# Kernel tuning notes

Measured on AMD Instinct MI355X. Metric: run time of the kernel, lower is better.

Reference implementation:

```python
import jax, jax.numpy as jnp
import numpy as np

B, N1, K, E, H = 64, 8, 128, 256, 512


def setup_inputs() -> dict:
    key = jax.random.key(0)
    ks = jax.random.split(key, 10)
    s = 1.0 / np.sqrt(E)
    sh = 1.0 / np.sqrt(H)
    return {
        "queries": jax.random.normal(ks[0], (B, N1, E), jnp.float32),
        "keys": jax.random.normal(ks[1], (B, N1, K, E), jnp.float32),
        "cum_subs_masks": jax.random.randint(ks[2], (B, N1, K, 1), 0, 2, jnp.int32),
        "num_neg": N1 - 1,
        "wk_w": jax.random.uniform(ks[3], (H, E), jnp.float32, -s, s),
        "wk_b": jax.random.uniform(ks[4], (H,), jnp.float32, -s, s),
        "wq_w": jax.random.uniform(ks[5], (H, E), jnp.float32, -s, s),
        "wq_b": jax.random.uniform(ks[6], (H,), jnp.float32, -s, s),
        "wv_w": jax.random.uniform(ks[7], (1, H), jnp.float32, -sh, sh),
        "wv_b": jax.random.uniform(ks[8], (1,), jnp.float32, -sh, sh),
    }


def reference(queries, keys, cum_subs_masks, num_neg, wk_w, wk_b, wq_w, wq_b, wv_w, wv_b):
    # queries: (B, N1, E) -> project and broadcast over keys dim
    q_proj = jnp.einsum("bne,he->bnh", queries, wq_w) + wq_b        # (B, N1, H)
    k_proj = jnp.einsum("bnke,he->bnkh", keys, wk_w) + wk_b          # (B, N1, K, H)
    hidden = jnp.tanh(q_proj[:, :, None, :] + k_proj)                # (B, N1, K, H)
    scores = jnp.einsum("bnkh,oh->bnko", hidden, wv_w) + wv_b        # (B, N1, K, 1)
    scores = scores + cum_subs_masks.astype(scores.dtype) * (-1e9)
    attn_weight = jax.nn.softmax(scores, axis=-2)                    # over K
    attn_out = jnp.sum(attn_weight * keys, axis=-2)                  # (B, N1, E)
    return attn_out, attn_weight
```

## Files before the change

### kernel.cpp

```cpp
#include <hip/hip_runtime.h>
#include <hip/hip_bf16.h>

#define B_  64
#define N1_ 8
#define KK  128
#define EE  256
#define HH  512
#define BN  (B_ * N1_)

typedef __attribute__((ext_vector_type(8))) short short8;
typedef __attribute__((ext_vector_type(4))) float f32x4;

__device__ __forceinline__ short bfs(float f) {
  __hip_bfloat16 h = __float2bfloat16(f);
  return __builtin_bit_cast(short, h);
}

__device__ __forceinline__ float tanhf_fast(float x) {
  float e2 = __builtin_amdgcn_exp2f(2.8853900817779268f * x);
  return 1.0f - 2.0f * __builtin_amdgcn_rcpf(e2 + 1.0f);
}

__device__ __forceinline__ void gload16(const void* g, void* l) {
  __builtin_amdgcn_global_load_lds(
      (const __attribute__((address_space(1))) void*)g,
      (__attribute__((address_space(3))) void*)l, 16, 0, 0);
}

__global__ __launch_bounds__(256) void k_prep(
    const float* __restrict__ wk_w,
    const float* __restrict__ queries,
    const float* __restrict__ wq_w,
    const float* __restrict__ wq_b,
    const float* __restrict__ wk_b,
    unsigned short* __restrict__ wk_fr,
    float* __restrict__ qp) {
  const int bid = blockIdx.x, t = threadIdx.x;
  if (bid < 64) {
    const int g  = bid * 256 + t;
    const int h  = g >> 5;
    const int e0 = (g & 31) * 8;
    float4 x = *(const float4*)(wk_w + (size_t)h * EE + e0);
    float4 y = *(const float4*)(wk_w + (size_t)h * EE + e0 + 4);
    short8 f;
    f[0] = bfs(x.x); f[1] = bfs(x.y); f[2] = bfs(x.z); f[3] = bfs(x.w);
    f[4] = bfs(y.x); f[5] = bfs(y.y); f[6] = bfs(y.z); f[7] = bfs(y.w);
    const int ht = h >> 4, hl = h & 15;
    const int s = e0 >> 5, lg = (e0 >> 3) & 3;
    const int chunk = (ht * 8 + s) * 64 + lg * 16 + hl;
    *(short8*)(wk_fr + (size_t)chunk * 8) = f;
  } else {
    const int w = t >> 6, l = t & 63, lg = l >> 4, ll = l & 15;
    const int g2 = bid - 64;
    const int bn0 = (g2 >> 1) * 16;
    const int ht0 = (g2 & 1) * 16;
    short8 af[8];
    {
      const float* qr = queries + (size_t)(bn0 + ll) * EE + lg * 8;
      #pragma unroll
      for (int s = 0; s < 8; ++s) {
        float4 x = *(const float4*)(qr + s * 32);
        float4 y = *(const float4*)(qr + s * 32 + 4);
        short8 f;
        f[0] = bfs(x.x); f[1] = bfs(x.y); f[2] = bfs(x.z); f[3] = bfs(x.w);
        f[4] = bfs(y.x); f[5] = bfs(y.y); f[6] = bfs(y.z); f[7] = bfs(y.w);
        af[s] = f;
      }
    }
    #pragma unroll
    for (int i = 0; i < 4; ++i) {
      const int ht = ht0 + w * 4 + i;
      const float* bp = wq_w + (size_t)(ht * 16 + ll) * EE + lg * 8;
      f32x4 a = {0.f, 0.f, 0.f, 0.f};
      #pragma unroll
      for (int s = 0; s < 8; ++s) {
        float4 x = *(const float4*)(bp + s * 32);
        float4 y = *(const float4*)(bp + s * 32 + 4);
        short8 f;
        f[0] = bfs(x.x); f[1] = bfs(x.y); f[2] = bfs(x.z); f[3] = bfs(x.w);
        f[4] = bfs(y.x); f[5] = bfs(y.y); f[6] = bfs(y.z); f[7] = bfs(y.w);
        a = __builtin_amdgcn_mfma_f32_16x16x32_bf16(af[s], f, a, 0, 0, 0);
      }
      const int h = ht * 16 + ll;
      const float add = wq_b[h] + wk_b[h];
      #pragma unroll
      for (int r = 0; r < 4; ++r)
        qp[(size_t)(bn0 + lg * 4 + r) * HH + h] = a[r] + add;
    }
  }
}

__global__ __launch_bounds__(256, 2) void k_fused(
    const float* __restrict__ keys,
    const unsigned short* __restrict__ wk_fr,
    const float* __restrict__ wv_w,
    const float* __restrict__ qp,
    const int* __restrict__ masks,
    float* __restrict__ out) {
  const int t  = threadIdx.x;
  const int w  = t >> 6;
  const int l  = t & 63;
  const int lg = l >> 4;
  const int ll = l & 15;
  const int bn = blockIdx.x;

  __shared__ __align__(16) char bsm[2][8192];
  __shared__ float qb_s[HH];
  __shared__ float wv_s[HH];
  __shared__ float sc[KK];
  __shared__ float red[2];
  __shared__ float4 po4[4][64];

  qb_s[t]       = qp[(size_t)bn * HH + t];
  qb_s[t + 256] = qp[(size_t)bn * HH + t + 256];
  wv_s[t]       = wv_w[t];
  wv_s[t + 256] = wv_w[t + 256];

  const char* wkb = (const char*)wk_fr;
  gload16(wkb + (size_t)t * 16,        &bsm[0][w * 1024]);
  gload16(wkb + 4096 + (size_t)t * 16, &bsm[0][4096 + w * 1024]);

  short8 af0[8], af1[8];
  {
    const float* kp0 = keys + (size_t)(bn * KK + w * 32 + ll) * EE + lg * 8;
    const float* kp1 = kp0 + 16 * EE;
    #pragma unroll
    for (int s = 0; s < 8; ++s) {
      float4 x = *(const float4*)(kp0 + s * 32);
      float4 y = *(const float4*)(kp0 + s * 32 + 4);
      short8 f;
      f[0] = bfs(x.x); f[1] = bfs(x.y); f[2] = bfs(x.z); f[3] = bfs(x.w);
      f[4] = bfs(y.x); f[5] = bfs(y.y); f[6] = bfs(y.z); f[7] = bfs(y.w);
      af0[s] = f;
      x = *(const float4*)(kp1 + s * 32);
      y = *(const float4*)(kp1 + s * 32 + 4);
      f[0] = bfs(x.x); f[1] = bfs(x.y); f[2] = bfs(x.z); f[3] = bfs(x.w);
      f[4] = bfs(y.x); f[5] = bfs(y.y); f[6] = bfs(y.z); f[7] = bfs(y.w);
      af1[s] = f;
    }
  }
  __syncthreads();

  float p0[4] = {0.f, 0.f, 0.f, 0.f};
  float p1[4] = {0.f, 0.f, 0.f, 0.f};

  for (int i = 0; i < 32; ++i) {
    if (i < 31) {
      const char* src = wkb + (size_t)(i + 1) * 8192 + (size_t)t * 16;
      char* dst = &bsm[(i + 1) & 1][w * 1024];
      gload16(src, dst);
      gload16(src + 4096, dst + 4096);
    }
    const char* buf = bsm[i & 1];
    f32x4 a0 = {0.f, 0.f, 0.f, 0.f};
    f32x4 a1 = {0.f, 0.f, 0.f, 0.f};
    #pragma unroll
    for (int s = 0; s < 8; ++s) {
      short8 bfr = *(const short8*)(buf + s * 1024 + l * 16);
      a0 = __builtin_amdgcn_mfma_f32_16x16x32_bf16(af0[s], bfr, a0, 0, 0, 0);
      a1 = __builtin_amdgcn_mfma_f32_16x16x32_bf16(af1[s], bfr, a1, 0, 0, 0);
    }
    const int h = i * 16 + ll;
    const float qb = qb_s[h];
    const float wv = wv_s[h];
    #pragma unroll
    for (int r = 0; r < 4; ++r) {
      p0[r] += wv * tanhf_fast(a0[r] + qb);
      p1[r] += wv * tanhf_fast(a1[r] + qb);
    }
    __syncthreads();
  }

  #pragma unroll
  for (int r = 0; r < 4; ++r) {
    #pragma unroll
    for (int off = 1; off <= 8; off <<= 1) {
      p0[r] += __shfl_xor(p0[r], off, 64);
      p1[r] += __shfl_xor(p1[r], off, 64);
    }
  }
  if (ll == 0) {
    #pragma unroll
    for (int r = 0; r < 4; ++r) {
      sc[w * 32 + lg * 4 + r]      = p0[r];
      sc[w * 32 + 16 + lg * 4 + r] = p1[r];
    }
  }
  __syncthreads();

  if (t < KK) sc[t] += (float)masks[bn * KK + t] * (-1e9f);
  __syncthreads();
  if (t < 64) {
    float a = fmaxf(sc[t], sc[t + 64]);
    #pragma unroll
    for (int off = 32; off >= 1; off >>= 1) a = fmaxf(a, __shfl_xor(a, off, 64));
    if (t == 0) red[0] = a;
  }
  __syncthreads();
  const float m = red[0];
  if (t < KK) sc[t] = expf(sc[t] - m);
  __syncthreads();
  if (t < 64) {
    float a = sc[t] + sc[t + 64];
    #pragma unroll
    for (int off = 32; off >= 1; off >>= 1) a += __shfl_xor(a, off, 64);
    if (t == 0) red[1] = a;
  }
  __syncthreads();
  const float inv = 1.f / red[1];
  if (t < KK) {
    float wgt = sc[t] * inv;
    sc[t] = wgt;
    out[BN * EE + (size_t)bn * KK + t] = wgt;
  }
  __syncthreads();

  {
    const float4* kb4 = (const float4*)(keys + (size_t)bn * KK * EE);
    const int kh = t >> 6, ln = t & 63;
    float4 acc = {0.f, 0.f, 0.f, 0.f};
    #pragma unroll 4
    for (int k = 0; k < 32; ++k) {
      const float wgt = sc[kh * 32 + k];
      float4 kv = kb4[(size_t)(kh * 32 + k) * 64 + ln];
      acc.x += wgt * kv.x; acc.y += wgt * kv.y;
      acc.z += wgt * kv.z; acc.w += wgt * kv.w;
    }
    po4[kh][ln] = acc;
  }
  __syncthreads();
  if (t < 64) {
    float4 a = po4[0][t], b = po4[1][t], c = po4[2][t], d = po4[3][t];
    float4 r;
    r.x = a.x + b.x + c.x + d.x;
    r.y = a.y + b.y + c.y + d.y;
    r.z = a.z + b.z + c.z + d.z;
    r.w = a.w + b.w + c.w + d.w;
    *(float4*)(out + (size_t)bn * EE + t * 4) = r;
  }
}

extern "C" void kernel_launch(void* const* d_in, const int* in_sizes, int n_in,
                              void* d_out, int out_size, void* d_ws, size_t ws_size,
                              hipStream_t stream) {
  const float* queries = (const float*)d_in[0];
  const float* keys    = (const float*)d_in[1];
  const int*   masks   = (const int*)d_in[2];
  const float* wk_w = (const float*)d_in[4];
  const float* wk_b = (const float*)d_in[5];
  const float* wq_w = (const float*)d_in[6];
  const float* wq_b = (const float*)d_in[7];
  const float* wv_w = (const float*)d_in[8];

  float* out = (float*)d_out;
  float* qp  = (float*)d_ws;
  unsigned short* wk_fr = (unsigned short*)(qp + BN * HH);

  k_prep<<<128, 256, 0, stream>>>(wk_w, queries, wq_w, wq_b, wk_b, wk_fr, qp);
  k_fused<<<BN, 256, 0, stream>>>(keys, wk_fr, wv_w, qp, masks, out);
}
```

Measured before the change: 57.17 us.

## Triple-buffer weight tiles with one barrier per step; reuse bf16 key fragments for output

Changes the Wk tile pipeline from double-buffered with a full __syncthreads per iteration to a three-slot ring. Each step waits with an explicit vmcnt and a single s_barrier, and the MFMA section runs at raised wave priority. The final weighted sum over keys now reuses the bf16 key fragments already in registers instead of re-reading fp32 keys from global memory, using cross-lane shuffle reductions. This removes a second pass over keys, but the attention output is now computed from bf16-rounded keys, which lowers precision and adds shuffle work.

```diff
diff --git a/kernel.cpp b/kernel.cpp
--- a/kernel.cpp
+++ b/kernel.cpp
@@ -15,7 +15,10 @@
   __hip_bfloat16 h = __float2bfloat16(f);
   return __builtin_bit_cast(short, h);
 }
-
+__device__ __forceinline__ float bf2f(short s) {
+  unsigned int u = ((unsigned int)(unsigned short)s) << 16;
+  return __builtin_bit_cast(float, u);
+}
 __device__ __forceinline__ float tanhf_fast(float x) {
   float e2 = __builtin_amdgcn_exp2f(2.8853900817779268f * x);
   return 1.0f - 2.0f * __builtin_amdgcn_rcpf(e2 + 1.0f);
@@ -104,21 +107,17 @@
   const int ll = l & 15;
   const int bn = blockIdx.x;
 
-  __shared__ __align__(16) char bsm[2][8192];
+  __shared__ __align__(16) char bsm[3 * 8192];
   __shared__ float qb_s[HH];
   __shared__ float wv_s[HH];
   __shared__ float sc[KK];
   __shared__ float red[2];
-  __shared__ float4 po4[4][64];
+  __shared__ float po[4][256];
 
   qb_s[t]       = qp[(size_t)bn * HH + t];
   qb_s[t + 256] = qp[(size_t)bn * HH + t + 256];
   wv_s[t]       = wv_w[t];
   wv_s[t + 256] = wv_w[t + 256];
-
-  const char* wkb = (const char*)wk_fr;
-  gload16(wkb + (size_t)t * 16,        &bsm[0][w * 1024]);
-  gload16(wkb + 4096 + (size_t)t * 16, &bsm[0][4096 + w * 1024]);
 
   short8 af0[8], af1[8];
   {
@@ -141,35 +140,58 @@
   }
   __syncthreads();
 
+  const char* wkb = (const char*)wk_fr;
+
+#define STAGE(ti, off) {                                                     \
+    const char* s_ = wkb + (size_t)(ti) * 8192 + (size_t)t * 16;             \
+    char* d_ = bsm + (off) + w * 1024;                                       \
+    gload16(s_, d_);                                                         \
+    gload16(s_ + 4096, d_ + 4096); }
+
+  STAGE(0, 0);
+  STAGE(1, 8192);
+
   float p0[4] = {0.f, 0.f, 0.f, 0.f};
   float p1[4] = {0.f, 0.f, 0.f, 0.f};
-
-  for (int i = 0; i < 32; ++i) {
-    if (i < 31) {
-      const char* src = wkb + (size_t)(i + 1) * 8192 + (size_t)t * 16;
-      char* dst = &bsm[(i + 1) & 1][w * 1024];
-      gload16(src, dst);
-      gload16(src + 4096, dst + 4096);
-    }
-    const char* buf = bsm[i & 1];
-    f32x4 a0 = {0.f, 0.f, 0.f, 0.f};
-    f32x4 a1 = {0.f, 0.f, 0.f, 0.f};
-    #pragma unroll
-    for (int s = 0; s < 8; ++s) {
-      short8 bfr = *(const short8*)(buf + s * 1024 + l * 16);
-      a0 = __builtin_amdgcn_mfma_f32_16x16x32_bf16(af0[s], bfr, a0, 0, 0, 0);
-      a1 = __builtin_amdgcn_mfma_f32_16x16x32_bf16(af1[s], bfr, a1, 0, 0, 0);
-    }
-    const int h = i * 16 + ll;
-    const float qb = qb_s[h];
-    const float wv = wv_s[h];
-    #pragma unroll
-    for (int r = 0; r < 4; ++r) {
-      p0[r] += wv * tanhf_fast(a0[r] + qb);
-      p1[r] += wv * tanhf_fast(a1[r] + qb);
-    }
-    __syncthreads();
-  }
+  int off0 = 0, off1 = 8192, off2 = 16384;
+
+#define COMPUTE(roff, ii) {                                                  \
+    f32x4 a0 = {0.f, 0.f, 0.f, 0.f};                                         \
+    f32x4 a1 = {0.f, 0.f, 0.f, 0.f};                                         \
+    __builtin_amdgcn_s_setprio(1);                                           \
+    _Pragma("unroll") for (int s = 0; s < 8; ++s) {                          \
+      short8 bfr = *(const short8*)(bsm + (roff) + s * 1024 + l * 16);       \
+      a0 = __builtin_amdgcn_mfma_f32_16x16x32_bf16(af0[s], bfr, a0, 0, 0, 0);\
+      a1 = __builtin_amdgcn_mfma_f32_16x16x32_bf16(af1[s], bfr, a1, 0, 0, 0);\
+    }                                                                        \
+    __builtin_amdgcn_s_setprio(0);                                           \
+    const int h = (ii) * 16 + ll;                                            \
+    const float qb = qb_s[h];                                                \
+    const float wv = wv_s[h];                                                \
+    _Pragma("unroll") for (int r = 0; r < 4; ++r) {                          \
+      p0[r] += wv * tanhf_fast(a0[r] + qb);                                  \
+      p1[r] += wv * tanhf_fast(a1[r] + qb); } }
+
+  #pragma unroll 1
+  for (int i = 0; i < 30; ++i) {
+    asm volatile("s_waitcnt vmcnt(2)" ::: "memory");
+    __builtin_amdgcn_s_barrier();
+    __builtin_amdgcn_sched_barrier(0);
+    STAGE(i + 2, off2);
+    COMPUTE(off0, i);
+    int tmp = off0; off0 = off1; off1 = off2; off2 = tmp;
+  }
+  asm volatile("s_waitcnt vmcnt(2)" ::: "memory");
+  __builtin_amdgcn_s_barrier();
+  __builtin_amdgcn_sched_barrier(0);
+  COMPUTE(off0, 30);
+  { int tmp = off0; off0 = off1; off1 = off2; off2 = tmp; }
+  asm volatile("s_waitcnt vmcnt(0)" ::: "memory");
+  __builtin_amdgcn_s_barrier();
+  __builtin_amdgcn_sched_barrier(0);
+  COMPUTE(off0, 31);
+#undef COMPUTE
+#undef STAGE
 
   #pragma unroll
   for (int r = 0; r < 4; ++r) {
@@ -216,28 +238,30 @@
   __syncthreads();
 
   {
-    const float4* kb4 = (const float4*)(keys + (size_t)bn * KK * EE);
-    const int kh = t >> 6, ln = t & 63;
-    float4 acc = {0.f, 0.f, 0.f, 0.f};
-    #pragma unroll 4
-    for (int k = 0; k < 32; ++k) {
-      const float wgt = sc[kh * 32 + k];
-      float4 kv = kb4[(size_t)(kh * 32 + k) * 64 + ln];
-      acc.x += wgt * kv.x; acc.y += wgt * kv.y;
-      acc.z += wgt * kv.z; acc.w += wgt * kv.w;
-    }
-    po4[kh][ln] = acc;
-  }
-  __syncthreads();
-  if (t < 64) {
-    float4 a = po4[0][t], b = po4[1][t], c = po4[2][t], d = po4[3][t];
-    float4 r;
-    r.x = a.x + b.x + c.x + d.x;
-    r.y = a.y + b.y + c.y + d.y;
-    r.z = a.z + b.z + c.z + d.z;
-    r.w = a.w + b.w + c.w + d.w;
-    *(float4*)(out + (size_t)bn * EE + t * 4) = r;
-  }
+    const float wgt0 = sc[w * 32 + ll];
+    const float wgt1 = sc[w * 32 + 16 + ll];
+    #pragma unroll
+    for (int s = 0; s < 8; ++s) {
+      float pv[8];
+      #pragma unroll
+      for (int j = 0; j < 8; ++j)
+        pv[j] = wgt0 * bf2f(af0[s][j]) + wgt1 * bf2f(af1[s][j]);
+      #pragma unroll
+      for (int j = 0; j < 8; ++j) {
+        #pragma unroll
+        for (int off = 1; off <= 8; off <<= 1)
+          pv[j] += __shfl_xor(pv[j], off, 64);
+      }
+      if (ll == 0) {
+        float4 v0 = {pv[0], pv[1], pv[2], pv[3]};
+        float4 v1 = {pv[4], pv[5], pv[6], pv[7]};
+        *(float4*)(&po[w][lg * 8 + s * 32])     = v0;
+        *(float4*)(&po[w][lg * 8 + s * 32 + 4]) = v1;
+      }
+    }
+  }
+  __syncthreads();
+  out[(size_t)bn * EE + t] = po[0][t] + po[1][t] + po[2][t] + po[3][t];
 }
 
 extern "C" void kernel_launch(void* const* d_in, const int* in_sizes, int n_in,
```

Result: faster. 55.76 us (-2.5%).

## Split fused attention into H-quartered scores kernel and separate softmax/output kernel

Applied to the files above, without the earlier changes.

Replaces the single fused kernel with two. The new scores kernel launches four blocks per (b,n) row, each covering a quarter of H: it copies that quarter's 64KB of bf16 Wk fragments into LDS once, then runs without the per-step double buffering and barriers. Partial scores go to a workspace buffer. A second kernel sums the partials, applies the mask and softmax, and computes the weighted key sum with 512 threads. This adds parallelism and removes per-iteration syncs. In exchange, each key tile is loaded and converted four times, there is one more launch and a workspace round trip, and the 64KB LDS use limits how many blocks fit on a CU.

```diff
diff --git a/kernel.cpp b/kernel.cpp
--- a/kernel.cpp
+++ b/kernel.cpp
@@ -15,16 +15,9 @@
   __hip_bfloat16 h = __float2bfloat16(f);
   return __builtin_bit_cast(short, h);
 }
-
 __device__ __forceinline__ float tanhf_fast(float x) {
   float e2 = __builtin_amdgcn_exp2f(2.8853900817779268f * x);
   return 1.0f - 2.0f * __builtin_amdgcn_rcpf(e2 + 1.0f);
-}
-
-__device__ __forceinline__ void gload16(const void* g, void* l) {
-  __builtin_amdgcn_global_load_lds(
-      (const __attribute__((address_space(1))) void*)g,
-      (__attribute__((address_space(3))) void*)l, 16, 0, 0);
 }
 
 __global__ __launch_bounds__(256) void k_prep(
@@ -90,105 +83,98 @@
   }
 }
 
-__global__ __launch_bounds__(256, 2) void k_fused(
+__global__ __launch_bounds__(512, 4) void k_scores(
     const float* __restrict__ keys,
     const unsigned short* __restrict__ wk_fr,
     const float* __restrict__ wv_w,
     const float* __restrict__ qp,
-    const int* __restrict__ masks,
-    float* __restrict__ out) {
+    float* __restrict__ scp) {
   const int t  = threadIdx.x;
   const int w  = t >> 6;
   const int l  = t & 63;
   const int lg = l >> 4;
   const int ll = l & 15;
-  const int bn = blockIdx.x;
-
-  __shared__ __align__(16) char bsm[2][8192];
-  __shared__ float qb_s[HH];
-  __shared__ float wv_s[HH];
-  __shared__ float sc[KK];
-  __shared__ float red[2];
-  __shared__ float4 po4[4][64];
-
-  qb_s[t]       = qp[(size_t)bn * HH + t];
-  qb_s[t + 256] = qp[(size_t)bn * HH + t + 256];
-  wv_s[t]       = wv_w[t];
-  wv_s[t + 256] = wv_w[t + 256];
-
-  const char* wkb = (const char*)wk_fr;
-  gload16(wkb + (size_t)t * 16,        &bsm[0][w * 1024]);
-  gload16(wkb + 4096 + (size_t)t * 16, &bsm[0][4096 + w * 1024]);
-
-  short8 af0[8], af1[8];
+  const int bid = blockIdx.x;
+  const int bn  = bid >> 2;
+  const int q   = bid & 3;
+
+  __shared__ __align__(16) char bq[8 * 8192];
+  __shared__ float2 qw_s[128];
+
   {
-    const float* kp0 = keys + (size_t)(bn * KK + w * 32 + ll) * EE + lg * 8;
-    const float* kp1 = kp0 + 16 * EE;
+    const float4* src = (const float4*)((const char*)wk_fr + (size_t)q * 8 * 8192);
+    float4* dst = (float4*)bq;
+    #pragma unroll
+    for (int j = 0; j < 8; ++j) dst[t + j * 512] = src[t + j * 512];
+  }
+  if (t < 128) {
+    float2 v; v.x = qp[(size_t)bn * HH + q * 128 + t]; v.y = wv_w[q * 128 + t];
+    qw_s[t] = v;
+  }
+
+  short8 af[8];
+  {
+    const float* kp = keys + (size_t)(bn * KK + w * 16 + ll) * EE + lg * 8;
     #pragma unroll
     for (int s = 0; s < 8; ++s) {
-      float4 x = *(const float4*)(kp0 + s * 32);
-      float4 y = *(const float4*)(kp0 + s * 32 + 4);
+      float4 x = *(const float4*)(kp + s * 32);
+      float4 y = *(const float4*)(kp + s * 32 + 4);
       short8 f;
       f[0] = bfs(x.x); f[1] = bfs(x.y); f[2] = bfs(x.z); f[3] = bfs(x.w);
       f[4] = bfs(y.x); f[5] = bfs(y.y); f[6] = bfs(y.z); f[7] = bfs(y.w);
-      af0[s] = f;
-      x = *(const float4*)(kp1 + s * 32);
-      y = *(const float4*)(kp1 + s * 32 + 4);
-      f[0] = bfs(x.x); f[1] = bfs(x.y); f[2] = bfs(x.z); f[3] = bfs(x.w);
-      f[4] = bfs(y.x); f[5] = bfs(y.y); f[6] = bfs(y.z); f[7] = bfs(y.w);
-      af1[s] = f;
-    }
-  }
-  __syncthreads();
-
-  float p0[4] = {0.f, 0.f, 0.f, 0.f};
-  float p1[4] = {0.f, 0.f, 0.f, 0.f};
-
-  for (int i = 0; i < 32; ++i) {
-    if (i < 31) {
-      const char* src = wkb + (size_t)(i + 1) * 8192 + (size_t)t * 16;
-      char* dst = &bsm[(i + 1) & 1][w * 1024];
-      gload16(src, dst);
-      gload16(src + 4096, dst + 4096);
-    }
-    const char* buf = bsm[i & 1];
+      af[s] = f;
+    }
+  }
+  __syncthreads();
+
+  float p[4] = {0.f, 0.f, 0.f, 0.f};
+
+  #pragma unroll
+  for (int i = 0; i < 8; ++i) {
+    const char* bt = bq + i * 8192;
     f32x4 a0 = {0.f, 0.f, 0.f, 0.f};
     f32x4 a1 = {0.f, 0.f, 0.f, 0.f};
     #pragma unroll
-    for (int s = 0; s < 8; ++s) {
-      short8 bfr = *(const short8*)(buf + s * 1024 + l * 16);
-      a0 = __builtin_amdgcn_mfma_f32_16x16x32_bf16(af0[s], bfr, a0, 0, 0, 0);
-      a1 = __builtin_amdgcn_mfma_f32_16x16x32_bf16(af1[s], bfr, a1, 0, 0, 0);
-    }
-    const int h = i * 16 + ll;
-    const float qb = qb_s[h];
-    const float wv = wv_s[h];
-    #pragma unroll
-    for (int r = 0; r < 4; ++r) {
-      p0[r] += wv * tanhf_fast(a0[r] + qb);
-      p1[r] += wv * tanhf_fast(a1[r] + qb);
-    }
-    __syncthreads();
+    for (int s = 0; s < 4; ++s) {
+      short8 b0 = *(const short8*)(bt + s * 1024 + l * 16);
+      short8 b1 = *(const short8*)(bt + (s + 4) * 1024 + l * 16);
+      a0 = __builtin_amdgcn_mfma_f32_16x16x32_bf16(af[s], b0, a0, 0, 0, 0);
+      a1 = __builtin_amdgcn_mfma_f32_16x16x32_bf16(af[s + 4], b1, a1, 0, 0, 0);
+    }
+    const float2 qw = qw_s[i * 16 + ll];
+    #pragma unroll
+    for (int r = 0; r < 4; ++r)
+      p[r] += qw.y * tanhf_fast(a0[r] + a1[r] + qw.x);
   }
 
   #pragma unroll
   for (int r = 0; r < 4; ++r) {
     #pragma unroll
-    for (int off = 1; off <= 8; off <<= 1) {
-      p0[r] += __shfl_xor(p0[r], off, 64);
-      p1[r] += __shfl_xor(p1[r], off, 64);
-    }
+    for (int off = 1; off <= 8; off <<= 1)
+      p[r] += __shfl_xor(p[r], off, 64);
   }
   if (ll == 0) {
     #pragma unroll
-    for (int r = 0; r < 4; ++r) {
-      sc[w * 32 + lg * 4 + r]      = p0[r];
-      sc[w * 32 + 16 + lg * 4 + r] = p1[r];
-    }
-  }
-  __syncthreads();
-
-  if (t < KK) sc[t] += (float)masks[bn * KK + t] * (-1e9f);
+    for (int r = 0; r < 4; ++r)
+      scp[(size_t)(bn * KK + w * 16 + lg * 4 + r) * 4 + q] = p[r];
+  }
+}
+
+__global__ __launch_bounds__(512) void k_smout(
+    const float* __restrict__ keys,
+    const int* __restrict__ masks,
+    const float* __restrict__ scp,
+    float* __restrict__ out) {
+  const int bn = blockIdx.x;
+  const int t  = threadIdx.x;
+  __shared__ float sc[KK];
+  __shared__ float4 po4[8][64];
+  __shared__ float red[2];
+
+  if (t < KK) {
+    float4 s4 = ((const float4*)scp)[(size_t)bn * KK + t];
+    sc[t] = s4.x + s4.y + s4.z + s4.w + (float)masks[bn * KK + t] * (-1e9f);
+  }
   __syncthreads();
   if (t < 64) {
     float a = fmaxf(sc[t], sc[t + 64]);
@@ -220,9 +206,9 @@
     const int kh = t >> 6, ln = t & 63;
     float4 acc = {0.f, 0.f, 0.f, 0.f};
     #pragma unroll 4
-    for (int k = 0; k < 32; ++k) {
-      const float wgt = sc[kh * 32 + k];
-      float4 kv = kb4[(size_t)(kh * 32 + k) * 64 + ln];
+    for (int k = 0; k < 16; ++k) {
+      const float wgt = sc[kh * 16 + k];
+      float4 kv = kb4[(size_t)(kh * 16 + k) * 64 + ln];
       acc.x += wgt * kv.x; acc.y += wgt * kv.y;
       acc.z += wgt * kv.z; acc.w += wgt * kv.w;
     }
@@ -230,12 +216,12 @@
   }
   __syncthreads();
   if (t < 64) {
-    float4 a = po4[0][t], b = po4[1][t], c = po4[2][t], d = po4[3][t];
-    float4 r;
-    r.x = a.x + b.x + c.x + d.x;
-    r.y = a.y + b.y + c.y + d.y;
-    r.z = a.z + b.z + c.z + d.z;
-    r.w = a.w + b.w + c.w + d.w;
+    float4 r = po4[0][t];
+    #pragma unroll
+    for (int g = 1; g < 8; ++g) {
+      float4 a = po4[g][t];
+      r.x += a.x; r.y += a.y; r.z += a.z; r.w += a.w;
+    }
     *(float4*)(out + (size_t)bn * EE + t * 4) = r;
   }
 }
@@ -255,7 +241,9 @@
   float* out = (float*)d_out;
   float* qp  = (float*)d_ws;
   unsigned short* wk_fr = (unsigned short*)(qp + BN * HH);
+  float* scp = (float*)(wk_fr + HH * EE);
 
   k_prep<<<128, 256, 0, stream>>>(wk_w, queries, wq_w, wq_b, wk_b, wk_fr, qp);
-  k_fused<<<BN, 256, 0, stream>>>(keys, wk_fr, wv_w, qp, masks, out);
-}
+  k_scores<<<BN * 4, 512, 0, stream>>>(keys, wk_fr, wv_w, qp, scp);
+  k_smout<<<BN, 512, 0, stream>>>(keys, masks, scp, out);
+}
```

After: 72.12 us. +26.1%, slower.
